# Optimization experiments

Hardware: AMD Instinct MI355X
Metric: run time of the kernel (lower is better)

Reference implementation:

```python
import jax, jax.numpy as jnp
import numpy as np

N, M, D, OUT, K, L = 2048, 64, 64, 64, 3, 3  # meta-nodes, subgraph-nodes, channels, out, hops, layers
EPS = 1e-5


def setup_inputs() -> dict:
    key = jax.random.key(0)
    ks = jax.random.split(key, 6)
    x = jax.random.normal(ks[0], (N, M, D), dtype=jnp.float32)
    adj = jax.random.randint(ks[1], (N, N), 0, 2, dtype=jnp.int32)        # meta-graph adjacency
    sub_adj = jax.random.randint(ks[2], (M, M), 0, 2, dtype=jnp.int32)    # per-node subgraph adjacency
    # GCNConv params: (num_layers, k+1 convs per layer, D, D)
    W_convs = jax.random.normal(ks[3], (L, K + 1, D, D), dtype=jnp.float32) / np.float32(np.sqrt(D))
    b_convs = jnp.zeros((L, K + 1, D), dtype=jnp.float32)
    # LayerNorm over the trailing (m, d) dims, per layer
    ln_gamma = jnp.ones((L, M, D), dtype=jnp.float32)
    ln_beta = jnp.zeros((L, M, D), dtype=jnp.float32)
    W_lin = jax.random.normal(ks[4], (M * D, OUT), dtype=jnp.float32) / np.float32(np.sqrt(M * D))
    b_lin = jnp.zeros((OUT,), dtype=jnp.float32)
    return dict(x=x, sub_adj=sub_adj, adj=adj, W_convs=W_convs, b_convs=b_convs,
                ln_gamma=ln_gamma, ln_beta=ln_beta, W_lin=W_lin, b_lin=b_lin)


def _gcn_norm(A):
    # symmetric GCN normalization with self loops: D^{-1/2} (A+I) D^{-1/2}
    A = A.astype(jnp.float32) + jnp.eye(A.shape[0], dtype=jnp.float32)
    dinv = jax.lax.rsqrt(A.sum(axis=1))  # degree >= 1 thanks to self loops
    return dinv[:, None] * A * dinv[None, :]


def reference(x, sub_adj, adj, W_convs, b_convs, ln_gamma, ln_beta, W_lin, b_lin):
    # precompute_adj: dense powers [A, A^2, ..., A^K] of the meta-graph adjacency
    A = adj.astype(jnp.float32)
    cached = [A]
    P = A
    for _ in range(K - 1):
        P = P @ A
        cached.append(P)

    Sn = _gcn_norm(sub_adj)  # (M, M) shared normalized subgraph propagation

    def gcn(h, W, b):
        # GCNConv over the subgraph (m) dimension: Sn @ (h W) + b, batched over n
        return jnp.einsum('uv,nvd->nud', Sn, h @ W) + b

    for l in range(L):
        h = gcn(x, W_convs[l, 0], b_convs[l, 0])  # L[0](x, sub_adj)
        x_i = x
        for i in range(K):
            # k-hop propagation over the meta graph: x_i <- A^i-power @ x_i
            x_i = jnp.einsum('nj,jmd->nmd', cached[i], x_i)
            h = h + gcn(x_i, W_convs[l, i + 1], b_convs[l, i + 1])
        # LayerNorm over trailing (m, d) dims, then ReLU
        mu = h.mean(axis=(1, 2), keepdims=True)
        var = h.var(axis=(1, 2), keepdims=True)
        x = (h - mu) * jax.lax.rsqrt(var + EPS) * ln_gamma[l] + ln_beta[l]
        x = jax.nn.relu(x)

    # final readout linear over flattened (m*d)
    out = x.reshape(N, M * D) @ W_lin + b_lin  # (N, OUT)
    return out
```

## Files before the change

kernel.cpp:

```cpp
#include <hip/hip_runtime.h>
#include <math.h>

#define NN 2048
#define MM 64
#define DD 64
#define MD 4096
#define NLAYER 3
#define EPS 1e-5f

typedef unsigned short u16;
typedef unsigned int u32;
typedef unsigned long long u64;
typedef __attribute__((ext_vector_type(8))) short bf16x8;
typedef __attribute__((ext_vector_type(4))) float f32x4;

__device__ inline u16 f32_to_bf16(float f) {
    u32 u = __float_as_uint(f);
    u32 r = (u + 0x7FFFu + ((u >> 16) & 1u)) >> 16;
    return (u16)r;
}
__device__ inline float bf16_to_f32(u16 h) { return __uint_as_float((u32)h << 16); }
__device__ inline void split3(float f, u16& h, u16& l, u16& q) {
    h = f32_to_bf16(f); float r = f - bf16_to_f32(h);
    l = f32_to_bf16(r); r -= bf16_to_f32(l);
    q = f32_to_bf16(r);
}

__global__ __launch_bounds__(256) void aprep_kernel(const int* __restrict__ adj,
                                                    u16* __restrict__ Abf,
                                                    u16* __restrict__ ATbf) {
    __shared__ u16 T[64][65];
    const int r0 = blockIdx.y * 64, c0 = blockIdx.x * 64;
    const int tid = threadIdx.x;
#pragma unroll
    for (int e = 0; e < 16; ++e) {
        int idx = e * 256 + tid;
        int i = idx >> 6, j = idx & 63;
        int a = adj[(long)(r0 + i) * NN + c0 + j];
        u16 b = a ? (u16)0x3F80 : (u16)0;
        Abf[(long)(r0 + i) * NN + c0 + j] = b;
        T[i][j] = b;
    }
    __syncthreads();
#pragma unroll
    for (int e = 0; e < 16; ++e) {
        int idx = e * 256 + tid;
        int cc = idx >> 6, rr = idx & 63;
        ATbf[(long)(c0 + cc) * NN + r0 + rr] = T[rr][cc];
    }
}

__global__ __launch_bounds__(256) void snprep_kernel(const int* __restrict__ sub,
                                                     u16* __restrict__ SnS) {
    __shared__ float dinv[64];
    __shared__ float Snl[64][65];
    int tid = threadIdx.x;
    if (tid < 64) {
        float s = 1.f;
        for (int v = 0; v < 64; ++v) s += (float)sub[tid * 64 + v];
        dinv[tid] = 1.f / sqrtf(s);
    }
    __syncthreads();
    for (int t = tid; t < 4096; t += 256) {
        int u = t >> 6, v = t & 63;
        float a = (float)sub[t] + (u == v ? 1.f : 0.f);
        Snl[u][v] = dinv[u] * a * dinv[v];
    }
    __syncthreads();
    for (int u = tid * 2; u < tid * 2 + 2; ++u) {
        int row = u >> 3, c8 = u & 7;
        int su = (u ^ ((u >> 3) & 7)) * 8;
#pragma unroll
        for (int e = 0; e < 8; ++e) {
            u16 h, l, q; split3(Snl[row][c8 * 8 + e], h, l, q);
            SnS[su + e] = h;
            SnS[4096 + su + e] = l;
            SnS[8192 + su + e] = q;
        }
    }
}

__global__ __launch_bounds__(256) void wprep_kernel(const float* __restrict__ Wc,
                                                    u16* __restrict__ WtS) {
    __shared__ float Wl[64][65];
    const int cu = blockIdx.x, tid = threadIdx.x;
    const float* W = Wc + (size_t)cu * 4096;
    for (int t = tid; t < 4096; t += 256) Wl[t >> 6][t & 63] = W[t];
    __syncthreads();
    u16* dst = WtS + (size_t)cu * 3 * 4096;
    for (int u = tid * 2; u < tid * 2 + 2; ++u) {
        int d = u >> 3, c8 = u & 7;
        int su = (u ^ ((u >> 3) & 7)) * 8;
#pragma unroll
        for (int e = 0; e < 8; ++e) {
            u16 h, l, q; split3(Wl[c8 * 8 + e][d], h, l, q);
            dst[su + e] = h;
            dst[4096 + su + e] = l;
            dst[8192 + su + e] = q;
        }
    }
}

__global__ __launch_bounds__(256) void split3t_kernel(const float* __restrict__ X,
                                                      u16* __restrict__ P, int R, int Cc) {
    __shared__ float T[64][65];
    const int r0 = blockIdx.y * 64, c0 = blockIdx.x * 64;
    const int tid = threadIdx.x;
#pragma unroll
    for (int e = 0; e < 16; ++e) {
        int idx = e * 256 + tid;
        int i = idx >> 6, j = idx & 63;
        T[i][j] = X[(long)(r0 + i) * Cc + c0 + j];
    }
    __syncthreads();
    const long planeStride = (long)R * Cc;
#pragma unroll
    for (int e = 0; e < 16; ++e) {
        int idx = e * 256 + tid;
        int cc = idx >> 6, rr = idx & 63;
        float v = T[rr][cc];
        u16 h, l, q; split3(v, h, l, q);
        long o = (long)(c0 + cc) * R + r0 + rr;
        P[o] = h;
        P[planeStride + o] = l;
        P[2 * planeStride + o] = q;
    }
}

template <int SP, int SQ, int SMAX, int OSPL, int OTRANS>
__global__ __launch_bounds__(256) void gemm_pairs(const u16* __restrict__ Ap, long aStride,
                                                  const u16* __restrict__ Bp, long bStride,
                                                  float* __restrict__ C,
                                                  u16* __restrict__ Sout,
                                                  int M, int N, int K) {
    __shared__ u16 lds[(SP + SQ) * 4096];
    const int tid = threadIdx.x;
    const int wave = tid >> 6, lane = tid & 63;
    const int nwg = gridDim.x * gridDim.y;
    int bid = blockIdx.y * gridDim.x + blockIdx.x;
    int sbid = (bid & 7) * (nwg >> 3) + (bid >> 3);
    const int bm = (sbid / gridDim.x) * 128, bn = (sbid % gridDim.x) * 128;
    const int wr = (wave >> 1) * 64, wc = (wave & 1) * 64;

    f32x4 acc[4][4];
#pragma unroll
    for (int i = 0; i < 4; ++i)
#pragma unroll
        for (int j = 0; j < 4; ++j) acc[i][j] = (f32x4){0.f, 0.f, 0.f, 0.f};

    const int kb16 = lane >> 4, lr = lane & 15;
    const int lg = lane >> 4;
    int aoff[4], boff[4];
#pragma unroll
    for (int mi = 0; mi < 4; ++mi) {
        int ua = (wr + mi * 16 + lr) * 4 + kb16;
        aoff[mi] = (ua ^ ((ua >> 3) & 7)) * 16;
        int ub = (wc + mi * 16 + lr) * 4 + kb16;
        boff[mi] = (ub ^ ((ub >> 3) & 7)) * 16;
    }
    auto stage = [&](int k0) {
#pragma unroll
        for (int u8 = 0; u8 < (SP + SQ) * 2; ++u8) {
            int uu = u8 * 4 + wave;
            int p = uu >> 3, i = uu & 7;
            int us = i * 64 + lane;
            int ulin = us ^ ((us >> 3) & 7);
            int r = ulin >> 2, kb = ulin & 3;
            const u16* src; int rowbase;
            if (p < SP) { src = Ap + (long)p * aStride; rowbase = bm; }
            else        { src = Bp + (long)(p - SP) * bStride; rowbase = bn; }
            const char* g = (const char*)src + ((long)(rowbase + r) * K + k0) * 2 + kb * 16;
            char* l = (char*)lds + p * 8192 + i * 1024 + lane * 16;
            __builtin_amdgcn_global_load_lds((const __attribute__((address_space(1))) void*)g,
                                             (__attribute__((address_space(3))) void*)l, 16, 0, 0);
        }
    };
    stage(0);
    __syncthreads();
    for (int k0 = 0; k0 < K; k0 += 32) {
        bf16x8 a[SP][4], b[SQ][4];
#pragma unroll
        for (int s = 0; s < SP; ++s)
#pragma unroll
            for (int mi = 0; mi < 4; ++mi)
                a[s][mi] = *(const bf16x8*)((const char*)lds + s * 8192 + aoff[mi]);
#pragma unroll
        for (int t = 0; t < SQ; ++t)
#pragma unroll
            for (int ni = 0; ni < 4; ++ni)
                b[t][ni] = *(const bf16x8*)((const char*)lds + (SP + t) * 8192 + boff[ni]);
        __syncthreads();
        if (k0 + 32 < K) stage(k0 + 32);
#pragma unroll
        for (int s = 0; s < SP; ++s)
#pragma unroll
            for (int t = 0; t < SQ; ++t)
                if (s + t <= SMAX) {
#pragma unroll
                    for (int mi = 0; mi < 4; ++mi)
#pragma unroll
                        for (int ni = 0; ni < 4; ++ni)
                            acc[mi][ni] = __builtin_amdgcn_mfma_f32_16x16x32_bf16(
                                a[s][mi], b[t][ni], acc[mi][ni], 0, 0, 0);
                }
        __syncthreads();
    }
#pragma unroll
    for (int mi = 0; mi < 4; ++mi)
#pragma unroll
        for (int ni = 0; ni < 4; ++ni)
#pragma unroll
            for (int j = 0; j < 4; ++j)
                C[(long)(bm + wr + mi * 16 + lg * 4 + j) * N + bn + wc + ni * 16 + lr] =
                    acc[mi][ni][j];
    if (OSPL > 0) {
        const long pe = (long)M * N;
        if (OTRANS) {
#pragma unroll
            for (int ni = 0; ni < 4; ++ni) {
                long col = bn + wc + ni * 16 + lr;
#pragma unroll
                for (int mi = 0; mi < 4; ++mi) {
                    long row0 = bm + wr + mi * 16 + lg * 4;
                    u16 hh[4], ll[4], qq[4];
#pragma unroll
                    for (int j = 0; j < 4; ++j) split3(acc[mi][ni][j], hh[j], ll[j], qq[j]);
                    long o = col * M + row0;
                    *(u64*)(Sout + o) =
                        (u64)hh[0] | ((u64)hh[1] << 16) | ((u64)hh[2] << 32) | ((u64)hh[3] << 48);
                    if (OSPL > 1)
                        *(u64*)(Sout + pe + o) =
                            (u64)ll[0] | ((u64)ll[1] << 16) | ((u64)ll[2] << 32) | ((u64)ll[3] << 48);
                    if (OSPL > 2)
                        *(u64*)(Sout + 2 * pe + o) =
                            (u64)qq[0] | ((u64)qq[1] << 16) | ((u64)qq[2] << 32) | ((u64)qq[3] << 48);
                }
            }
        } else {
#pragma unroll
            for (int mi = 0; mi < 4; ++mi)
#pragma unroll
                for (int j = 0; j < 4; ++j) {
                    long row = bm + wr + mi * 16 + lg * 4 + j;
#pragma unroll
                    for (int ni = 0; ni < 4; ++ni) {
                        long o = row * N + bn + wc + ni * 16 + lr;
                        u16 h, l, q; split3(acc[mi][ni][j], h, l, q);
                        Sout[o] = h;
                        if (OSPL > 1) Sout[pe + o] = l;
                        if (OSPL > 2) Sout[2 * pe + o] = q;
                    }
                }
        }
    }
}

template <int NC, int MODE>
__global__ __launch_bounds__(256, 2) void gcn_conv_kernel(
    const float* __restrict__ X0, const float* __restrict__ X1,
    const float* __restrict__ X2, const float* __restrict__ X3,
    const u16* __restrict__ WtS,
    const float* __restrict__ bias,
    const u16* __restrict__ SnS,
    const float* __restrict__ gam, const float* __restrict__ bet,
    float* __restrict__ Hout) {
    __shared__ u16 lds[9 * 4096];
    __shared__ float redf[4];
    const int tid = threadIdx.x;
    const int wave = tid >> 6, lane = tid & 63;
    const int lr = lane & 15, lg = lane >> 4;
    const int n = blockIdx.x;
    const int TT = 0, WT = 3 * 4096, SN = 6 * 4096;

    {
        const char* src = (const char*)SnS;
        char* dst = (char*)lds + (size_t)SN * 2;
#pragma unroll
        for (int i = 0; i < 6; ++i)
            __builtin_amdgcn_global_load_lds(
                (const __attribute__((address_space(1))) void*)(src + (i * 256 + tid) * 16),
                (__attribute__((address_space(3))) void*)(dst + (i * 256 + tid) * 16), 16, 0, 0);
    }
    const float* Xc[4] = {X0, X1, X2, X3};
    f32x4 accH[4];
#pragma unroll
    for (int ni = 0; ni < 4; ++ni) accH[ni] = (f32x4){0.f, 0.f, 0.f, 0.f};

    for (int c = 0; c < NC; ++c) {
        __syncthreads();
        {
            const char* wsrc = (const char*)(WtS + (size_t)c * 3 * 4096);
            char* wdst = (char*)lds + (size_t)WT * 2;
#pragma unroll
            for (int i = 0; i < 6; ++i)
                __builtin_amdgcn_global_load_lds(
                    (const __attribute__((address_space(1))) void*)(wsrc + (i * 256 + tid) * 16),
                    (__attribute__((address_space(3))) void*)(wdst + (i * 256 + tid) * 16), 16, 0, 0);
        }
        const float* xp = Xc[c] + (size_t)n * 4096;
        bf16x8 xb[3][4][2];
#pragma unroll
        for (int ni = 0; ni < 4; ++ni)
#pragma unroll
            for (int ks = 0; ks < 2; ++ks) {
                int off = (ni * 16 + lr) * 64 + ks * 32 + lg * 8;
                f32x4 v0 = *(const f32x4*)(xp + off);
                f32x4 v1 = *(const f32x4*)(xp + off + 4);
#pragma unroll
                for (int e = 0; e < 8; ++e) {
                    float f = (e < 4) ? v0[e] : v1[e - 4];
                    u16 h, l, q; split3(f, h, l, q);
                    xb[0][ni][ks][e] = (short)h;
                    xb[1][ni][ks][e] = (short)l;
                    xb[2][ni][ks][e] = (short)q;
                }
            }
        __syncthreads();
        f32x4 accT[4];
#pragma unroll
        for (int ni = 0; ni < 4; ++ni) accT[ni] = (f32x4){0.f, 0.f, 0.f, 0.f};
#pragma unroll
        for (int ks = 0; ks < 2; ++ks) {
            bf16x8 aw[3];
#pragma unroll
            for (int s = 0; s < 3; ++s) {
                int u = (wave * 16 + lr) * 8 + ks * 4 + lg;
                aw[s] = *(const bf16x8*)(lds + WT + s * 4096 + (u ^ ((u >> 3) & 7)) * 8);
            }
#pragma unroll
            for (int ni = 0; ni < 4; ++ni) {
                accT[ni] = __builtin_amdgcn_mfma_f32_16x16x32_bf16(aw[0], xb[0][ni][ks], accT[ni], 0, 0, 0);
                accT[ni] = __builtin_amdgcn_mfma_f32_16x16x32_bf16(aw[0], xb[1][ni][ks], accT[ni], 0, 0, 0);
                accT[ni] = __builtin_amdgcn_mfma_f32_16x16x32_bf16(aw[1], xb[0][ni][ks], accT[ni], 0, 0, 0);
                accT[ni] = __builtin_amdgcn_mfma_f32_16x16x32_bf16(aw[1], xb[1][ni][ks], accT[ni], 0, 0, 0);
                accT[ni] = __builtin_amdgcn_mfma_f32_16x16x32_bf16(aw[2], xb[0][ni][ks], accT[ni], 0, 0, 0);
                accT[ni] = __builtin_amdgcn_mfma_f32_16x16x32_bf16(aw[0], xb[2][ni][ks], accT[ni], 0, 0, 0);
            }
        }
#pragma unroll
        for (int ni = 0; ni < 4; ++ni)
#pragma unroll
            for (int j = 0; j < 4; ++j) {
                int d = wave * 16 + lg * 4 + j;
                int v = ni * 16 + lr;
                u16 h, l, q; split3(accT[ni][j], h, l, q);
                int u = d * 8 + (v >> 3);
                int o = (u ^ ((u >> 3) & 7)) * 8 + (v & 7);
                lds[TT + o] = h;
                lds[TT + 4096 + o] = l;
                lds[TT + 8192 + o] = q;
            }
        __syncthreads();
#pragma unroll
        for (int ks = 0; ks < 2; ++ks) {
            bf16x8 as_[3];
#pragma unroll
            for (int s = 0; s < 3; ++s) {
                int u = (wave * 16 + lr) * 8 + ks * 4 + lg;
                as_[s] = *(const bf16x8*)(lds + SN + s * 4096 + (u ^ ((u >> 3) & 7)) * 8);
            }
#pragma unroll
            for (int ni = 0; ni < 4; ++ni) {
                bf16x8 bt[3];
#pragma unroll
                for (int t = 0; t < 3; ++t) {
                    int u = (ni * 16 + lr) * 8 + ks * 4 + lg;
                    bt[t] = *(const bf16x8*)(lds + TT + t * 4096 + (u ^ ((u >> 3) & 7)) * 8);
                }
                accH[ni] = __builtin_amdgcn_mfma_f32_16x16x32_bf16(as_[0], bt[0], accH[ni], 0, 0, 0);
                accH[ni] = __builtin_amdgcn_mfma_f32_16x16x32_bf16(as_[0], bt[1], accH[ni], 0, 0, 0);
                accH[ni] = __builtin_amdgcn_mfma_f32_16x16x32_bf16(as_[1], bt[0], accH[ni], 0, 0, 0);
                accH[ni] = __builtin_amdgcn_mfma_f32_16x16x32_bf16(as_[1], bt[1], accH[ni], 0, 0, 0);
                accH[ni] = __builtin_amdgcn_mfma_f32_16x16x32_bf16(as_[2], bt[0], accH[ni], 0, 0, 0);
                accH[ni] = __builtin_amdgcn_mfma_f32_16x16x32_bf16(as_[0], bt[2], accH[ni], 0, 0, 0);
            }
        }
#pragma unroll
        for (int ni = 0; ni < 4; ++ni) {
            float bv = bias[c * 64 + ni * 16 + lr];
            accH[ni][0] += bv; accH[ni][1] += bv; accH[ni][2] += bv; accH[ni][3] += bv;
        }
    }
    float* hp = Hout + (size_t)n * 4096;
    float val[4][4];
#pragma unroll
    for (int ni = 0; ni < 4; ++ni)
#pragma unroll
        for (int j = 0; j < 4; ++j) {
            int idx = (wave * 16 + lg * 4 + j) * 64 + ni * 16 + lr;
            float v = accH[ni][j];
            if (MODE == 0 || MODE == 2) v += hp[idx];
            val[ni][j] = v;
        }
    if (MODE == 0 || MODE == 1) {
#pragma unroll
        for (int ni = 0; ni < 4; ++ni)
#pragma unroll
            for (int j = 0; j < 4; ++j)
                hp[(wave * 16 + lg * 4 + j) * 64 + ni * 16 + lr] = val[ni][j];
        return;
    }
    float part = 0.f;
#pragma unroll
    for (int ni = 0; ni < 4; ++ni)
#pragma unroll
        for (int j = 0; j < 4; ++j) part += val[ni][j];
#pragma unroll
    for (int o = 32; o; o >>= 1) part += __shfl_down(part, o);
    if (lane == 0) redf[wave] = part;
    __syncthreads();
    float mean = (redf[0] + redf[1] + redf[2] + redf[3]) * (1.f / 4096.f);
    float p2 = 0.f;
#pragma unroll
    for (int ni = 0; ni < 4; ++ni)
#pragma unroll
        for (int j = 0; j < 4; ++j) {
            float d_ = val[ni][j] - mean;
            p2 += d_ * d_;
        }
#pragma unroll
    for (int o = 32; o; o >>= 1) p2 += __shfl_down(p2, o);
    __syncthreads();
    if (lane == 0) redf[wave] = p2;
    __syncthreads();
    float var = (redf[0] + redf[1] + redf[2] + redf[3]) * (1.f / 4096.f);
    float rstd = 1.f / sqrtf(var + EPS);
#pragma unroll
    for (int ni = 0; ni < 4; ++ni)
#pragma unroll
        for (int j = 0; j < 4; ++j) {
            int idx = (wave * 16 + lg * 4 + j) * 64 + ni * 16 + lr;
            float v = (val[ni][j] - mean) * rstd * gam[idx] + bet[idx];
            hp[idx] = v > 0.f ? v : 0.f;
        }
}

__global__ __launch_bounds__(256) void readout_kernel(const float* __restrict__ X,
                                                      const float* __restrict__ Wl,
                                                      const float* __restrict__ bl,
                                                      float* __restrict__ out) {
    __shared__ float Wls[64][64];
    __shared__ float red[4][8][64];
    const int tid = threadIdx.x;
    const int o = tid & 63, c = tid >> 6;
    const int n0 = blockIdx.x * 8;
    float acc[8] = {};
    const int r = tid >> 2, cq = (tid & 3) * 16;
    for (int k0 = 0; k0 < 4096; k0 += 64) {
        __syncthreads();
        const float* wsrc = Wl + (long)(k0 + r) * 64 + cq;
        *(f32x4*)&Wls[r][cq + 0]  = *(const f32x4*)(wsrc + 0);
        *(f32x4*)&Wls[r][cq + 4]  = *(const f32x4*)(wsrc + 4);
        *(f32x4*)&Wls[r][cq + 8]  = *(const f32x4*)(wsrc + 8);
        *(f32x4*)&Wls[r][cq + 12] = *(const f32x4*)(wsrc + 12);
        __syncthreads();
#pragma unroll
        for (int i = 0; i < 8; ++i) {
            const float* xr = X + (long)(n0 + i) * 4096 + k0 + c * 16;
            float s = acc[i];
#pragma unroll
            for (int kk = 0; kk < 16; ++kk) s += xr[kk] * Wls[c * 16 + kk][o];
            acc[i] = s;
        }
    }
#pragma unroll
    for (int i = 0; i < 8; ++i) red[c][i][o] = acc[i];
    __syncthreads();
    if (c == 0) {
#pragma unroll
        for (int i = 0; i < 8; ++i)
            out[(long)(n0 + i) * 64 + o] =
                red[0][i][o] + red[1][i][o] + red[2][i][o] + red[3][i][o] + bl[o];
    }
}

extern "C" void kernel_launch(void* const* d_in, const int* in_sizes, int n_in,
                              void* d_out, int out_size, void* d_ws, size_t ws_size,
                              hipStream_t stream) {
    const float* x     = (const float*)d_in[0];
    const int*   sub   = (const int*)d_in[1];
    const int*   adj   = (const int*)d_in[2];
    const float* Wc    = (const float*)d_in[3];
    const float* bc    = (const float*)d_in[4];
    const float* gamma = (const float*)d_in[5];
    const float* beta  = (const float*)d_in[6];
    const float* Wlin  = (const float*)d_in[7];
    const float* blin  = (const float*)d_in[8];
    float* out = (float*)d_out;

    char* w = (char*)d_ws;
    u16* Abf = (u16*)w;  w += (size_t)NN * NN * 2;
    u16* A2p = (u16*)w;  w += (size_t)2 * NN * NN * 2;
    u16* A3p = (u16*)w;  w += (size_t)3 * NN * NN * 2;
    u16* SnS = (u16*)w;  w += (size_t)3 * 4096 * 2;
    u16* WtS = (u16*)w;  w += (size_t)12 * 3 * 4096 * 2;
    const size_t baseBytes = (size_t)(w - (char*)d_ws);
    const size_t sbytes = (size_t)3 * NN * MD * 2;
    const size_t ybytes = (size_t)NN * MD * 4;
    const long sPlane = (long)NN * MD;

    u16* S0 = (u16*)w;
    u16* ATbf = S0;

    const size_t needA = baseBytes + 2 * sbytes + 4 * ybytes;
    const size_t needB = baseBytes + 2 * sbytes + 3 * ybytes;
    int tier = (ws_size >= needA) ? 0 : (ws_size >= needB) ? 1 : 2;

    float* Cscr = (tier == 2) ? (float*)((char*)S0 + sbytes)
                              : (float*)((char*)S0 + 2 * sbytes);

    aprep_kernel<<<dim3(32, 32), 256, 0, stream>>>(adj, Abf, ATbf);
    snprep_kernel<<<1, 256, 0, stream>>>(sub, SnS);
    wprep_kernel<<<12, 256, 0, stream>>>(Wc, WtS);
    gemm_pairs<1, 1, 2, 2, 0><<<dim3(16, 16), 256, 0, stream>>>(
        Abf, 0, ATbf, 0, Cscr, A2p, NN, NN, NN);
    gemm_pairs<2, 1, 2, 3, 0><<<dim3(16, 16), 256, 0, stream>>>(
        A2p, (long)NN * NN, ATbf, 0, Cscr, A3p, NN, NN, NN);

    const dim3 gp(32, 16);
    if (tier == 0) {
        u16* S1 = S0 + (size_t)3 * sPlane;
        float* Y[4];
        char* yw = (char*)S1 + sbytes;
        for (int i = 0; i < 4; ++i) { Y[i] = (float*)yw; yw += ybytes; }
        const float* xin = x;
        for (int l = 0; l < NLAYER; ++l) {
            float* p1 = Y[l % 4];
            float* p2 = Y[(l + 1) % 4];
            float* p3 = Y[(l + 2) % 4];
            const u16* Wl = WtS + (size_t)l * 12 * 4096;
            split3t_kernel<<<dim3(64, 32), 256, 0, stream>>>(xin, S0, NN, MD);
            gemm_pairs<1, 3, 2, 3, 1><<<gp, 256, 0, stream>>>(
                Abf, 0, S0, sPlane, p1, S1, NN, MD, NN);
            gemm_pairs<2, 3, 2, 3, 1><<<gp, 256, 0, stream>>>(
                A2p, (long)NN * NN, S1, sPlane, p2, S0, NN, MD, NN);
            gemm_pairs<3, 3, 2, 0, 0><<<gp, 256, 0, stream>>>(
                A3p, (long)NN * NN, S0, sPlane, p3, nullptr, NN, MD, NN);
            gcn_conv_kernel<4, 3><<<NN, 256, 0, stream>>>(xin, p1, p2, p3, Wl,
                bc + (size_t)l * 256, SnS, gamma + (size_t)l * 4096, beta + (size_t)l * 4096, p1);
            xin = p1;
        }
        readout_kernel<<<NN / 8, 256, 0, stream>>>(xin, Wlin, blin, out);
    } else if (tier == 1) {
        u16* S1 = S0 + (size_t)3 * sPlane;
        char* yw = (char*)S1 + sbytes;
        float* Xa = (float*)yw; yw += ybytes;
        float* Ha = (float*)yw; yw += ybytes;
        float* Hb = (float*)yw; yw += ybytes;
        const float* xin = x;
        for (int l = 0; l < NLAYER; ++l) {
            float* H = (l & 1) ? Hb : Ha;
            const u16* Wl = WtS + (size_t)l * 12 * 4096;
            const float* bl = bc + (size_t)l * 256;
            split3t_kernel<<<dim3(64, 32), 256, 0, stream>>>(xin, S0, NN, MD);
            gcn_conv_kernel<1, 1><<<NN, 256, 0, stream>>>(xin, xin, xin, xin, Wl, bl,
                SnS, nullptr, nullptr, H);
            gemm_pairs<1, 3, 2, 3, 1><<<gp, 256, 0, stream>>>(
                Abf, 0, S0, sPlane, Xa, S1, NN, MD, NN);
            gcn_conv_kernel<1, 0><<<NN, 256, 0, stream>>>(Xa, Xa, Xa, Xa, Wl + 3 * 4096, bl + 64,
                SnS, nullptr, nullptr, H);
            gemm_pairs<2, 3, 2, 3, 1><<<gp, 256, 0, stream>>>(
                A2p, (long)NN * NN, S1, sPlane, Xa, S0, NN, MD, NN);
            gcn_conv_kernel<1, 0><<<NN, 256, 0, stream>>>(Xa, Xa, Xa, Xa, Wl + 6 * 4096, bl + 128,
                SnS, nullptr, nullptr, H);
            gemm_pairs<3, 3, 2, 0, 0><<<gp, 256, 0, stream>>>(
                A3p, (long)NN * NN, S0, sPlane, Xa, nullptr, NN, MD, NN);
            gcn_conv_kernel<1, 2><<<NN, 256, 0, stream>>>(Xa, Xa, Xa, Xa, Wl + 9 * 4096, bl + 192,
                SnS, gamma + (size_t)l * 4096, beta + (size_t)l * 4096, H);
            xin = H;
        }
        readout_kernel<<<NN / 8, 256, 0, stream>>>(xin, Wlin, blin, out);
    } else {
        char* yw = (char*)S0 + sbytes;
        float* Xp = (float*)yw; yw += ybytes;
        float* H  = (float*)yw; yw += ybytes;
        const float* xin = x;
        for (int l = 0; l < NLAYER; ++l) {
            const u16* Wl = WtS + (size_t)l * 12 * 4096;
            const float* bl = bc + (size_t)l * 256;
            split3t_kernel<<<dim3(64, 32), 256, 0, stream>>>(xin, S0, NN, MD);
            gemm_pairs<1, 3, 2, 0, 0><<<gp, 256, 0, stream>>>(
                Abf, 0, S0, sPlane, Xp, nullptr, NN, MD, NN);
            gcn_conv_kernel<1, 1><<<NN, 256, 0, stream>>>(xin, xin, xin, xin, Wl, bl,
                SnS, nullptr, nullptr, H);
            gcn_conv_kernel<1, 0><<<NN, 256, 0, stream>>>(Xp, Xp, Xp, Xp, Wl + 3 * 4096, bl + 64,
                SnS, nullptr, nullptr, H);
            split3t_kernel<<<dim3(64, 32), 256, 0, stream>>>(Xp, S0, NN, MD);
            gemm_pairs<2, 3, 2, 0, 0><<<gp, 256, 0, stream>>>(
                A2p, (long)NN * NN, S0, sPlane, Xp, nullptr, NN, MD, NN);
            gcn_conv_kernel<1, 0><<<NN, 256, 0, stream>>>(Xp, Xp, Xp, Xp, Wl + 6 * 4096, bl + 128,
                SnS, nullptr, nullptr, H);
            split3t_kernel<<<dim3(64, 32), 256, 0, stream>>>(Xp, S0, NN, MD);
            gemm_pairs<3, 3, 2, 0, 0><<<gp, 256, 0, stream>>>(
                A3p, (long)NN * NN, S0, sPlane, Xp, nullptr, NN, MD, NN);
            gcn_conv_kernel<1, 2><<<NN, 256, 0, stream>>>(Xp, Xp, Xp, Xp, Wl + 9 * 4096, bl + 192,
                SnS, gamma + (size_t)l * 4096, beta + (size_t)l * 4096, H);
            xin = H;
        }
        readout_kernel<<<NN / 8, 256, 0, stream>>>(xin, Wlin, blin, out);
    }
}
```

Baseline: 1.925 ms.

## Load A operand fragments directly from global into registers with prefetch

After: 2.533 ms. 31.6% more time.

```diff
diff --git a/kernel.cpp b/kernel.cpp
--- a/kernel.cpp
+++ b/kernel.cpp
@@ -128,12 +128,12 @@
 }
 
 template <int SP, int SQ, int SMAX, int OSPL, int OTRANS>
-__global__ __launch_bounds__(256) void gemm_pairs(const u16* __restrict__ Ap, long aStride,
-                                                  const u16* __restrict__ Bp, long bStride,
-                                                  float* __restrict__ C,
-                                                  u16* __restrict__ Sout,
-                                                  int M, int N, int K) {
-    __shared__ u16 lds[(SP + SQ) * 4096];
+__global__ __launch_bounds__(256, 2) void gemm_pairs(const u16* __restrict__ Ap, long aStride,
+                                                     const u16* __restrict__ Bp, long bStride,
+                                                     float* __restrict__ C,
+                                                     u16* __restrict__ Sout,
+                                                     int M, int N, int K) {
+    __shared__ u16 lds[SQ * 4096];
     const int tid = threadIdx.x;
     const int wave = tid >> 6, lane = tid & 63;
     const int nwg = gridDim.x * gridDim.y;
@@ -150,47 +150,61 @@
 
     const int kb16 = lane >> 4, lr = lane & 15;
     const int lg = lane >> 4;
-    int aoff[4], boff[4];
-#pragma unroll
-    for (int mi = 0; mi < 4; ++mi) {
-        int ua = (wr + mi * 16 + lr) * 4 + kb16;
-        aoff[mi] = (ua ^ ((ua >> 3) & 7)) * 16;
-        int ub = (wc + mi * 16 + lr) * 4 + kb16;
-        boff[mi] = (ub ^ ((ub >> 3) & 7)) * 16;
-    }
-    auto stage = [&](int k0) {
-#pragma unroll
-        for (int u8 = 0; u8 < (SP + SQ) * 2; ++u8) {
+    int boff[4];
+#pragma unroll
+    for (int ni = 0; ni < 4; ++ni) {
+        int ub = (wc + ni * 16 + lr) * 4 + kb16;
+        boff[ni] = (ub ^ ((ub >> 3) & 7)) * 16;
+    }
+    const u16* aBase[3];
+#pragma unroll
+    for (int s = 0; s < SP; ++s)
+        aBase[s] = Ap + (long)s * aStride + (long)(bm + wr + lr) * K + kb16 * 8;
+
+    auto stageB = [&](int k0) {
+#pragma unroll
+        for (int u8 = 0; u8 < SQ * 2; ++u8) {
             int uu = u8 * 4 + wave;
             int p = uu >> 3, i = uu & 7;
             int us = i * 64 + lane;
             int ulin = us ^ ((us >> 3) & 7);
             int r = ulin >> 2, kb = ulin & 3;
-            const u16* src; int rowbase;
-            if (p < SP) { src = Ap + (long)p * aStride; rowbase = bm; }
-            else        { src = Bp + (long)(p - SP) * bStride; rowbase = bn; }
-            const char* g = (const char*)src + ((long)(rowbase + r) * K + k0) * 2 + kb * 16;
+            const char* g = (const char*)(Bp + (long)p * bStride) +
+                            ((long)(bn + r) * K + k0) * 2 + kb * 16;
             char* l = (char*)lds + p * 8192 + i * 1024 + lane * 16;
             __builtin_amdgcn_global_load_lds((const __attribute__((address_space(1))) void*)g,
                                              (__attribute__((address_space(3))) void*)l, 16, 0, 0);
         }
     };
-    stage(0);
+
+    bf16x8 areg[SP][4];
+#pragma unroll
+    for (int s = 0; s < SP; ++s)
+#pragma unroll
+        for (int mi = 0; mi < 4; ++mi)
+            areg[s][mi] = *(const bf16x8*)(aBase[s] + (long)mi * 16 * K);
+
+    stageB(0);
     __syncthreads();
     for (int k0 = 0; k0 < K; k0 += 32) {
-        bf16x8 a[SP][4], b[SQ][4];
-#pragma unroll
-        for (int s = 0; s < SP; ++s)
-#pragma unroll
-            for (int mi = 0; mi < 4; ++mi)
-                a[s][mi] = *(const bf16x8*)((const char*)lds + s * 8192 + aoff[mi]);
+        bf16x8 b[SQ][4];
 #pragma unroll
         for (int t = 0; t < SQ; ++t)
 #pragma unroll
             for (int ni = 0; ni < 4; ++ni)
-                b[t][ni] = *(const bf16x8*)((const char*)lds + (SP + t) * 8192 + boff[ni]);
+                b[t][ni] = *(const bf16x8*)((const char*)lds + t * 8192 + boff[ni]);
+        bf16x8 anext[SP][4];
+        const bool more = (k0 + 32 < K);
+        if (more) {
+#pragma unroll
+            for (int s = 0; s < SP; ++s)
+#pragma unroll
+                for (int mi = 0; mi < 4; ++mi)
+                    anext[s][mi] = *(const bf16x8*)(aBase[s] + (long)mi * 16 * K + k0 + 32);
+        }
         __syncthreads();
-        if (k0 + 32 < K) stage(k0 + 32);
+        if (more) stageB(k0 + 32);
+        __builtin_amdgcn_s_setprio(1);
 #pragma unroll
         for (int s = 0; s < SP; ++s)
 #pragma unroll
@@ -201,8 +215,16 @@
 #pragma unroll
                         for (int ni = 0; ni < 4; ++ni)
                             acc[mi][ni] = __builtin_amdgcn_mfma_f32_16x16x32_bf16(
-                                a[s][mi], b[t][ni], acc[mi][ni], 0, 0, 0);
+                                areg[s][mi], b[t][ni], acc[mi][ni], 0, 0, 0);
                 }
+        __builtin_amdgcn_s_setprio(0);
+        if (more) {
+#pragma unroll
+            for (int s = 0; s < SP; ++s)
+#pragma unroll
+                for (int mi = 0; mi < 4; ++mi)
+                    areg[s][mi] = anext[s][mi];
+        }
         __syncthreads();
     }
 #pragma unroll
```

## Widen GEMM tiles to 128x256 with 512-thread blocks and MFMA priority

Applied to the files above, without the earlier changes.

Measured after the change: 6.279 ms. +226.3%, slower.

```diff
diff --git a/kernel.cpp b/kernel.cpp
--- a/kernel.cpp
+++ b/kernel.cpp
@@ -128,19 +128,23 @@
 }
 
 template <int SP, int SQ, int SMAX, int OSPL, int OTRANS>
-__global__ __launch_bounds__(256) void gemm_pairs(const u16* __restrict__ Ap, long aStride,
-                                                  const u16* __restrict__ Bp, long bStride,
-                                                  float* __restrict__ C,
-                                                  u16* __restrict__ Sout,
-                                                  int M, int N, int K) {
-    __shared__ u16 lds[(SP + SQ) * 4096];
+__global__ __launch_bounds__(512, 4) void gemm_pairs(const u16* __restrict__ Ap, long aStride,
+                                                     const u16* __restrict__ Bp, long bStride,
+                                                     float* __restrict__ C,
+                                                     u16* __restrict__ Sout,
+                                                     int M, int N, int K) {
+    constexpr int ABYTES = SP * 8192;
+    constexpr int BBYTES = SQ * 16384;
+    __shared__ char lds[ABYTES + BBYTES];
     const int tid = threadIdx.x;
     const int wave = tid >> 6, lane = tid & 63;
     const int nwg = gridDim.x * gridDim.y;
     int bid = blockIdx.y * gridDim.x + blockIdx.x;
     int sbid = (bid & 7) * (nwg >> 3) + (bid >> 3);
-    const int bm = (sbid / gridDim.x) * 128, bn = (sbid % gridDim.x) * 128;
-    const int wr = (wave >> 1) * 64, wc = (wave & 1) * 64;
+    const int bm = (sbid / gridDim.x) * 128;
+    const int bn = (sbid % gridDim.x) * 256;
+    const int wr = (wave >> 2) * 64, wc = (wave & 3) * 64;
+    const int lr = lane & 15, kb16 = lane >> 4, lg = lane >> 4;
 
     f32x4 acc[4][4];
 #pragma unroll
@@ -148,33 +152,45 @@
 #pragma unroll
         for (int j = 0; j < 4; ++j) acc[i][j] = (f32x4){0.f, 0.f, 0.f, 0.f};
 
-    const int kb16 = lane >> 4, lr = lane & 15;
-    const int lg = lane >> 4;
     int aoff[4], boff[4];
 #pragma unroll
     for (int mi = 0; mi < 4; ++mi) {
         int ua = (wr + mi * 16 + lr) * 4 + kb16;
         aoff[mi] = (ua ^ ((ua >> 3) & 7)) * 16;
-        int ub = (wc + mi * 16 + lr) * 4 + kb16;
-        boff[mi] = (ub ^ ((ub >> 3) & 7)) * 16;
-    }
+    }
+#pragma unroll
+    for (int ni = 0; ni < 4; ++ni) {
+        int ub = (wc + ni * 16 + lr) * 4 + kb16;
+        boff[ni] = (ub ^ ((ub >> 3) & 7)) * 16;
+    }
+
     auto stage = [&](int k0) {
 #pragma unroll
-        for (int u8 = 0; u8 < (SP + SQ) * 2; ++u8) {
-            int uu = u8 * 4 + wave;
-            int p = uu >> 3, i = uu & 7;
-            int us = i * 64 + lane;
-            int ulin = us ^ ((us >> 3) & 7);
+        for (int p = 0; p < SP; ++p) {
+            int ulin = tid ^ ((tid >> 3) & 7);
             int r = ulin >> 2, kb = ulin & 3;
-            const u16* src; int rowbase;
-            if (p < SP) { src = Ap + (long)p * aStride; rowbase = bm; }
-            else        { src = Bp + (long)(p - SP) * bStride; rowbase = bn; }
-            const char* g = (const char*)src + ((long)(rowbase + r) * K + k0) * 2 + kb * 16;
-            char* l = (char*)lds + p * 8192 + i * 1024 + lane * 16;
-            __builtin_amdgcn_global_load_lds((const __attribute__((address_space(1))) void*)g,
-                                             (__attribute__((address_space(3))) void*)l, 16, 0, 0);
-        }
+            const char* g = (const char*)(Ap + (long)p * aStride) +
+                            ((long)(bm + r) * K + k0) * 2 + kb * 16;
+            __builtin_amdgcn_global_load_lds(
+                (const __attribute__((address_space(1))) void*)g,
+                (__attribute__((address_space(3))) void*)(lds + p * 8192 + tid * 16), 16, 0, 0);
+        }
+#pragma unroll
+        for (int t = 0; t < SQ; ++t)
+#pragma unroll
+            for (int h = 0; h < 2; ++h) {
+                int us = h * 512 + tid;
+                int ulin = us ^ ((us >> 3) & 7);
+                int r = ulin >> 2, kb = ulin & 3;
+                const char* g = (const char*)(Bp + (long)t * bStride) +
+                                ((long)(bn + r) * K + k0) * 2 + kb * 16;
+                __builtin_amdgcn_global_load_lds(
+                    (const __attribute__((address_space(1))) void*)g,
+                    (__attribute__((address_space(3))) void*)(lds + ABYTES + t * 16384 + us * 16),
+                    16, 0, 0);
+            }
     };
+
     stage(0);
     __syncthreads();
     for (int k0 = 0; k0 < K; k0 += 32) {
@@ -183,14 +199,15 @@
         for (int s = 0; s < SP; ++s)
 #pragma unroll
             for (int mi = 0; mi < 4; ++mi)
-                a[s][mi] = *(const bf16x8*)((const char*)lds + s * 8192 + aoff[mi]);
+                a[s][mi] = *(const bf16x8*)(lds + s * 8192 + aoff[mi]);
 #pragma unroll
         for (int t = 0; t < SQ; ++t)
 #pragma unroll
             for (int ni = 0; ni < 4; ++ni)
-                b[t][ni] = *(const bf16x8*)((const char*)lds + (SP + t) * 8192 + boff[ni]);
+                b[t][ni] = *(const bf16x8*)(lds + ABYTES + t * 16384 + boff[ni]);
         __syncthreads();
         if (k0 + 32 < K) stage(k0 + 32);
+        __builtin_amdgcn_s_setprio(1);
 #pragma unroll
         for (int s = 0; s < SP; ++s)
 #pragma unroll
@@ -203,8 +220,10 @@
                             acc[mi][ni] = __builtin_amdgcn_mfma_f32_16x16x32_bf16(
                                 a[s][mi], b[t][ni], acc[mi][ni], 0, 0, 0);
                 }
+        __builtin_amdgcn_s_setprio(0);
         __syncthreads();
     }
+
 #pragma unroll
     for (int mi = 0; mi < 4; ++mi)
 #pragma unroll
@@ -512,12 +531,12 @@
     aprep_kernel<<<dim3(32, 32), 256, 0, stream>>>(adj, Abf, ATbf);
     snprep_kernel<<<1, 256, 0, stream>>>(sub, SnS);
     wprep_kernel<<<12, 256, 0, stream>>>(Wc, WtS);
-    gemm_pairs<1, 1, 2, 2, 0><<<dim3(16, 16), 256, 0, stream>>>(
+    gemm_pairs<1, 1, 2, 2, 0><<<dim3(8, 16), 512, 0, stream>>>(
         Abf, 0, ATbf, 0, Cscr, A2p, NN, NN, NN);
-    gemm_pairs<2, 1, 2, 3, 0><<<dim3(16, 16), 256, 0, stream>>>(
+    gemm_pairs<2, 1, 2, 3, 0><<<dim3(8, 16), 512, 0, stream>>>(
         A2p, (long)NN * NN, ATbf, 0, Cscr, A3p, NN, NN, NN);
 
-    const dim3 gp(32, 16);
+    const dim3 gp(16, 16);
     if (tier == 0) {
         u16* S1 = S0 + (size_t)3 * sPlane;
         float* Y[4];
@@ -530,11 +549,11 @@
             float* p3 = Y[(l + 2) % 4];
             const u16* Wl = WtS + (size_t)l * 12 * 4096;
             split3t_kernel<<<dim3(64, 32), 256, 0, stream>>>(xin, S0, NN, MD);
-            gemm_pairs<1, 3, 2, 3, 1><<<gp, 256, 0, stream>>>(
+            gemm_pairs<1, 3, 2, 3, 1><<<gp, 512, 0, stream>>>(
                 Abf, 0, S0, sPlane, p1, S1, NN, MD, NN);
-            gemm_pairs<2, 3, 2, 3, 1><<<gp, 256, 0, stream>>>(
+            gemm_pairs<2, 3, 2, 3, 1><<<gp, 512, 0, stream>>>(
                 A2p, (long)NN * NN, S1, sPlane, p2, S0, NN, MD, NN);
-            gemm_pairs<3, 3, 2, 0, 0><<<gp, 256, 0, stream>>>(
+            gemm_pairs<3, 3, 2, 0, 0><<<gp, 512, 0, stream>>>(
                 A3p, (long)NN * NN, S0, sPlane, p3, nullptr, NN, MD, NN);
             gcn_conv_kernel<4, 3><<<NN, 256, 0, stream>>>(xin, p1, p2, p3, Wl,
                 bc + (size_t)l * 256, SnS, gamma + (size_t)l * 4096, beta + (size_t)l * 4096, p1);
@@ -555,15 +574,15 @@
             split3t_kernel<<<dim3(64, 32), 256, 0, stream>>>(xin, S0, NN, MD);
             gcn_conv_kernel<1, 1><<<NN, 256, 0, stream>>>(xin, xin, xin, xin, Wl, bl,
                 SnS, nullptr, nullptr, H);
-            gemm_pairs<1, 3, 2, 3, 1><<<gp, 256, 0, stream>>>(
+            gemm_pairs<1, 3, 2, 3, 1><<<gp, 512, 0, stream>>>(
                 Abf, 0, S0, sPlane, Xa, S1, NN, MD, NN);
             gcn_conv_kernel<1, 0><<<NN, 256, 0, stream>>>(Xa, Xa, Xa, Xa, Wl + 3 * 4096, bl + 64,
                 SnS, nullptr, nullptr, H);
-            gemm_pairs<2, 3, 2, 3, 1><<<gp, 256, 0, stream>>>(
+            gemm_pairs<2, 3, 2, 3, 1><<<gp, 512, 0, stream>>>(
                 A2p, (long)NN * NN, S1, sPlane, Xa, S0, NN, MD, NN);
             gcn_conv_kernel<1, 0><<<NN, 256, 0, stream>>>(Xa, Xa, Xa, Xa, Wl + 6 * 4096, bl + 128,
                 SnS, nullptr, nullptr, H);
-            gemm_pairs<3, 3, 2, 0, 0><<<gp, 256, 0, stream>>>(
+            gemm_pairs<3, 3, 2, 0, 0><<<gp, 512, 0, stream>>>(
                 A3p, (long)NN * NN, S0, sPlane, Xa, nullptr, NN, MD, NN);
             gcn_conv_kernel<1, 2><<<NN, 256, 0, stream>>>(Xa, Xa, Xa, Xa, Wl + 9 * 4096, bl + 192,
                 SnS, gamma + (size_t)l * 4096, beta + (size_t)l * 4096, H);
@@ -579,19 +598,19 @@
             const u16* Wl = WtS + (size_t)l * 12 * 4096;
             const float* bl = bc + (size_t)l * 256;
             split3t_kernel<<<dim3(64, 32), 256, 0, stream>>>(xin, S0, NN, MD);
-            gemm_pairs<1, 3, 2, 0, 0><<<gp, 256, 0, stream>>>(
+            gemm_pairs<1, 3, 2, 0, 0><<<gp, 512, 0, stream>>>(
                 Abf, 0, S0, sPlane, Xp, nullptr, NN, MD, NN);
             gcn_conv_kernel<1, 1><<<NN, 256, 0, stream>>>(xin, xin, xin, xin, Wl, bl,
                 SnS, nullptr, nullptr, H);
             gcn_conv_kernel<1, 0><<<NN, 256, 0, stream>>>(Xp, Xp, Xp, Xp, Wl + 3 * 4096, bl + 64,
                 SnS, nullptr, nullptr, H);
             split3t_kernel<<<dim3(64, 32), 256, 0, stream>>>(Xp, S0, NN, MD);
-            gemm_pairs<2, 3, 2, 0, 0><<<gp, 256, 0, stream>>>(
+            gemm_pairs<2, 3, 2, 0, 0><<<gp, 512, 0, stream>>>(
                 A2p, (long)NN * NN, S0, sPlane, Xp, nullptr, NN, MD, NN);
             gcn_conv_kernel<1, 0><<<NN, 256, 0, stream>>>(Xp, Xp, Xp, Xp, Wl + 6 * 4096, bl + 128,
                 SnS, nullptr, nullptr, H);
             split3t_kernel<<<dim3(64, 32), 256, 0, stream>>>(Xp, S0, NN, MD);
-            gemm_pairs<3, 3, 2, 0, 0><<<gp, 256, 0, stream>>>(
+            gemm_pairs<3, 3, 2, 0, 0><<<gp, 512, 0, stream>>>(
                 A3p, (long)NN * NN, S0, sPlane, Xp, nullptr, NN, MD, NN);
             gcn_conv_kernel<1, 2><<<NN, 256, 0, stream>>>(Xp, Xp, Xp, Xp, Wl + 9 * 4096, bl + 192,
                 SnS, gamma + (size_t)l * 4096, beta + (size_t)l * 4096, H);
```
